# Performance work log

Measured on AMD Instinct MI355X. Metric: run time of the kernel, lower is better.

## Reference

```python
import jax, jax.numpy as jnp
import numpy as np

B, N, L, D, IN, H = 16, 100, 90, 300, 256, 256


def setup_inputs() -> dict:
    key = jax.random.key(0)
    ks = jax.random.split(key, 24)
    s = 0.02
    inp = {}
    inp["h_local"] = jax.random.normal(ks[0], (B, N, IN), jnp.float32)
    inp["items_review"] = jax.random.normal(ks[1], (B, N, L, D), jnp.float32)
    inp["adj_sg"] = jax.random.randint(ks[2], (B, N, 2 * N), 0, 2, jnp.int32)
    inp["attn_review_mask"] = jnp.zeros((B, N, L), jnp.bool_)
    # BatchNorm affine params (eval mode, running_mean=0, running_var=1)
    inp["bn_gamma"] = jnp.ones((IN,), jnp.float32)
    inp["bn_beta"] = jnp.zeros((IN,), jnp.float32)
    # MultiHeadAttention linear layers (review_dim=300)
    inp["W_q"] = jax.random.normal(ks[3], (D, D), jnp.float32) * s
    inp["b_q"] = jnp.zeros((D,), jnp.float32)
    inp["W_k"] = jax.random.normal(ks[4], (D, D), jnp.float32) * s
    inp["b_k"] = jnp.zeros((D,), jnp.float32)
    inp["W_v"] = jax.random.normal(ks[5], (D, D), jnp.float32) * s
    inp["b_v"] = jnp.zeros((D,), jnp.float32)
    inp["W_f"] = jax.random.normal(ks[6], (D, D), jnp.float32) * s
    inp["b_f"] = jnp.zeros((D,), jnp.float32)
    # fc: input_size -> hidden_size
    inp["W_fc"] = jax.random.normal(ks[7], (H, IN), jnp.float32) * s
    inp["b_fc"] = jnp.zeros((H,), jnp.float32)
    # edge linear layers
    inp["W_in"] = jax.random.normal(ks[8], (H, H), jnp.float32) * s
    inp["b_in"] = jnp.zeros((H,), jnp.float32)
    inp["W_out"] = jax.random.normal(ks[9], (H, H), jnp.float32) * s
    inp["b_out"] = jnp.zeros((H,), jnp.float32)
    inp["b_iah"] = jax.random.normal(ks[10], (H,), jnp.float32) * s
    inp["b_oah"] = jax.random.normal(ks[11], (H,), jnp.float32) * s
    # fc_in_out: 2H -> H
    inp["W_io"] = jax.random.normal(ks[12], (H, 2 * H), jnp.float32) * s
    inp["b_io"] = jnp.zeros((H,), jnp.float32)
    return inp


def reference(h_local, items_review, adj_sg, attn_review_mask,
              bn_gamma, bn_beta,
              W_q, b_q, W_k, b_k, W_v, b_v, W_f, b_f,
              W_fc, b_fc, W_in, b_in, W_out, b_out,
              b_iah, b_oah, W_io, b_io):
    n = h_local.shape[1]
    # BatchNorm1d (eval mode: running_mean=0, running_var=1) + fc
    h = h_local * (bn_gamma / jnp.sqrt(1.0 + 1e-5)) + bn_beta
    hidden = h @ W_fc.T + b_fc                                  # [B,N,H]

    # MultiHeadAttention over reviews (heads never split in original bmm)
    q = items_review @ W_q.T + b_q                              # [B,N,L,D]
    k = items_review @ W_k.T + b_k
    v = items_review @ W_v.T + b_v
    scale = (items_review.shape[-1] // 3) ** (-0.5)             # (300//3)^-0.5 = 0.1
    attn = jax.nn.softmax(jnp.einsum('bnld,bnmd->bnlm', q, k) * scale, axis=-1)
    ctx = jnp.einsum('bnlm,bnmd->bnld', attn, v)
    out_attn = items_review + (ctx @ W_f.T + b_f)               # residual
    h_review = jnp.sum(out_attn, axis=2)                        # [B,N,D] sum over review_len

    # pairwise cosine similarity (torch.cosine_similarity, eps=1e-8)
    norms = jnp.linalg.norm(h_review, axis=-1)                  # [B,N]
    sim = jnp.einsum('bnd,bmd->bnm', h_review, h_review) \
        / jnp.maximum(norms[:, :, None] * norms[:, None, :], 1e-8)

    adj_in = adj_sg[:, :, :n] > 0
    adj_out = adj_sg[:, :, n:2 * n] > 0
    NEG = jnp.float32(-9e15)
    sim_in = jax.nn.softmax(jnp.where(adj_in, sim, NEG), axis=-1)
    sim_out = jax.nn.softmax(jnp.where(adj_out, sim, NEG), axis=-1)

    input_in = jnp.einsum('bnm,bmh->bnh', sim_in, hidden @ W_in.T + b_in) + b_iah
    input_out = jnp.einsum('bnm,bmh->bnh', sim_out, hidden @ W_out.T + b_out) + b_oah
    output = jnp.concatenate([input_in, input_out], axis=-1) @ W_io.T + b_io
    return output
```

## Files before the change

### kernel.cpp

```cpp
#include <hip/hip_runtime.h>
#include <math.h>

#define Bb 16
#define Nn 100
#define Ll 90
#define Dd 300
#define NBLK (Bb*Nn)
#define LP 96
#define DP 320
#define DPH 40

typedef __attribute__((ext_vector_type(8))) short short8v;
typedef __attribute__((ext_vector_type(4))) short short4v;
typedef __attribute__((ext_vector_type(4))) float f32x4;

__device__ __forceinline__ unsigned short f2bf(float f) {
  unsigned int u = __float_as_uint(f);
  u += 0x7fffu + ((u >> 16) & 1u);
  return (unsigned short)(u >> 16);
}
__device__ __forceinline__ float bf2f(unsigned short h) {
  return __uint_as_float(((unsigned int)h) << 16);
}

__global__ __launch_bounds__(256) void k_setup(
    const float* __restrict__ Wq, const float* __restrict__ Wk,
    const float* __restrict__ bq, const float* __restrict__ bk,
    const float* __restrict__ Wf, const float* __restrict__ Wv,
    const float* __restrict__ bv, const float* __restrict__ bf,
    unsigned short* __restrict__ Mb, float* __restrict__ G,
    float* __restrict__ bias2) {
  int blk = blockIdx.x;
  if (blk < 400) {
    int idx = blk * 256 + threadIdx.x;
    int i = idx / DP, j = idx % DP;
    float s = 0.f;
    if (i <= Dd && j <= Dd) {
#pragma unroll 10
      for (int o = 0; o < Dd; o++) {
        float av = (i < Dd) ? Wq[o * Dd + i] : bq[o];
        float bw = (j < Dd) ? Wk[o * Dd + j] : bk[o];
        s += av * bw;
      }
    }
    Mb[idx] = f2bf(s);
  } else if (blk < 757) {
    int idx = (blk - 400) * 256 + threadIdx.x;
    if (idx < Dd * 304) {
      int o = idx / 304, p = idx % 304;
      float s = 0.f;
      if (p < Dd) {
#pragma unroll 10
        for (int v = 0; v < Dd; v++) s += Wf[o * Dd + v] * Wv[v * Dd + p];
      }
      G[idx] = s;
    }
  } else {
    for (int t = threadIdx.x; t < 304; t += 256) {
      float sb = 0.f;
      if (t < Dd) {
#pragma unroll 10
        for (int v = 0; v < Dd; v++) sb += Wf[t * Dd + v] * bv[v];
        sb = 90.f * (sb + bf[t]);
      }
      bias2[t] = sb;
    }
  }
}

__global__ __launch_bounds__(256) void k_mm256(
    const float* __restrict__ A0, const float* __restrict__ A1, int lda,
    const float* __restrict__ B0, const float* __restrict__ B1, int ldb,
    float* __restrict__ C, int ldc, const float* __restrict__ gamma) {
  const float* A = blockIdx.z ? A1 : A0;
  const float* B = blockIdx.z ? B1 : B0;
  float* Cb = C + (size_t)blockIdx.z * 256 * ldc;
  __shared__ float As[16][68];
  __shared__ float Bs[16][68];
  int m0 = blockIdx.x * 64, n0 = blockIdx.y * 64;
  int tx = threadIdx.x & 15, ty = threadIdx.x >> 4;
  float acc[4][4];
#pragma unroll
  for (int i = 0; i < 4; i++)
#pragma unroll
    for (int j = 0; j < 4; j++) acc[i][j] = 0.f;
  int r = threadIdx.x >> 2;
  int kq = (threadIdx.x & 3) << 2;
  int kk2 = threadIdx.x >> 4;
  int nq = (threadIdx.x & 15) << 2;
  for (int k0 = 0; k0 < 256; k0 += 16) {
    {
      float4 v = *(const float4*)(A + (size_t)(m0 + r) * lda + k0 + kq);
      As[kq + 0][r] = v.x; As[kq + 1][r] = v.y; As[kq + 2][r] = v.z; As[kq + 3][r] = v.w;
    }
    {
      float4 v = *(const float4*)(B + (size_t)(k0 + kk2) * ldb + n0 + nq);
      Bs[kk2][nq + 0] = v.x; Bs[kk2][nq + 1] = v.y; Bs[kk2][nq + 2] = v.z; Bs[kk2][nq + 3] = v.w;
    }
    __syncthreads();
#pragma unroll
    for (int kk = 0; kk < 16; kk++) {
      float4 av = *(const float4*)&As[kk][ty * 4];
      float4 bv = *(const float4*)&Bs[kk][tx * 4];
      acc[0][0] += av.x * bv.x; acc[0][1] += av.x * bv.y; acc[0][2] += av.x * bv.z; acc[0][3] += av.x * bv.w;
      acc[1][0] += av.y * bv.x; acc[1][1] += av.y * bv.y; acc[1][2] += av.y * bv.z; acc[1][3] += av.y * bv.w;
      acc[2][0] += av.z * bv.x; acc[2][1] += av.z * bv.y; acc[2][2] += av.z * bv.z; acc[2][3] += av.z * bv.w;
      acc[3][0] += av.w * bv.x; acc[3][1] += av.w * bv.y; acc[3][2] += av.w * bv.z; acc[3][3] += av.w * bv.w;
    }
    __syncthreads();
  }
  const float bninv = rsqrtf(1.00001f);
#pragma unroll
  for (int i = 0; i < 4; i++) {
    int gm = m0 + ty * 4 + i;
#pragma unroll
    for (int j = 0; j < 4; j++) {
      int gn = n0 + tx * 4 + j;
      float v = acc[i][j];
      if (gamma) v *= gamma[gn] * bninv;
      Cb[(size_t)gm * ldc + gn] = v;
    }
  }
}

__global__ __launch_bounds__(256) void k_vecd(
    const float* __restrict__ W_fc, const float* __restrict__ b_fc,
    const float* __restrict__ beta,
    const float* __restrict__ W_in, const float* __restrict__ b_in,
    const float* __restrict__ b_iah,
    const float* __restrict__ W_out, const float* __restrict__ b_out,
    const float* __restrict__ b_oah,
    const float* __restrict__ W_io, const float* __restrict__ b_io,
    float* __restrict__ dvec) {
  __shared__ float v1[256];
  __shared__ float v23[512];
  int i = threadIdx.x;
  float s = 0.f;
#pragma unroll 16
  for (int k = 0; k < 256; k++) s += W_fc[i * 256 + k] * beta[k];
  v1[i] = s + b_fc[i];
  __syncthreads();
  float s2 = 0.f, s3 = 0.f;
#pragma unroll 16
  for (int k = 0; k < 256; k++) {
    float vk = v1[k];
    s2 += W_in[i * 256 + k] * vk;
    s3 += W_out[i * 256 + k] * vk;
  }
  v23[i] = s2 + b_in[i] + b_iah[i];
  v23[256 + i] = s3 + b_out[i] + b_oah[i];
  __syncthreads();
  float sd = 0.f;
#pragma unroll 16
  for (int k = 0; k < 512; k++) sd += W_io[i * 512 + k] * v23[k];
  dvec[i] = sd + b_io[i];
}

__global__ __launch_bounds__(512, 4) void k_attn(
    const float* __restrict__ items, const unsigned short* __restrict__ Mb,
    float* __restrict__ r_all, float* __restrict__ colsum_all) {
  __shared__ unsigned short Xs[LP * DP];
  __shared__ unsigned short Zc[LP * 64];
  __shared__ float wsum[LP];

  const int tid = threadIdx.x;
  const int bid = blockIdx.x;
  const float* Xg = items + (size_t)bid * (Ll * Dd);

  if (tid < LP) wsum[tid] = 0.f;

  for (int c = tid; c < LP * DPH; c += 512) {
    int l = c / DPH, ch = c % DPH, d0 = ch * 8;
    float v[8];
    if (l < Ll && d0 < Dd) {
      if (d0 + 8 <= Dd) {
        float4 a = *(const float4*)(Xg + l * Dd + d0);
        float4 b = *(const float4*)(Xg + l * Dd + d0 + 4);
        v[0] = a.x; v[1] = a.y; v[2] = a.z; v[3] = a.w;
        v[4] = b.x; v[5] = b.y; v[6] = b.z; v[7] = b.w;
      } else {
#pragma unroll
        for (int q = 0; q < 8; q++) {
          int d = d0 + q;
          v[q] = (d < Dd) ? Xg[l * Dd + d] : ((d == Dd) ? 1.f : 0.f);
        }
      }
    } else {
#pragma unroll
      for (int q = 0; q < 8; q++) v[q] = 0.f;
    }
    short8v pk;
#pragma unroll
    for (int q = 0; q < 8; q++) pk[q] = (short)f2bf(v[q]);
    *(short8v*)((char*)Xs + l * 640 + ((d0 * 2) ^ ((l & 7) << 4))) = pk;
  }

  for (int d = tid; d < 304; d += 512) {
    float s = 0.f;
    if (d < Dd) {
#pragma unroll 18
      for (int l = 0; l < Ll; l++) s += Xg[l * Dd + d];
    }
    colsum_all[(size_t)bid * 304 + d] = s;
  }
  __syncthreads();

  const int lane = tid & 63, wave = tid >> 6;
  const int fr = lane & 15, kg = lane >> 4;

  int itile[3], bbyte[3], bswz[3], mrow[3], icol0[3];
#pragma unroll
  for (int tt = 0; tt < 3; tt++) {
    int t = wave + tt * 8;
    int ict = t / 6, mt = t - ict * 6;
    itile[tt] = ict * 16 + fr;
    int brow = mt * 16 + fr;
    bbyte[tt] = brow * 640;
    bswz[tt] = (brow & 7) << 4;
    mrow[tt] = brow;
    icol0[tt] = ict * 16 + kg * 4;
  }

  f32x4 acc[6];
#pragma unroll
  for (int mt = 0; mt < 6; mt++) acc[mt] = (f32x4){0.f, 0.f, 0.f, 0.f};

  for (int c = 0; c < 5; c++) {
    f32x4 z0 = (f32x4){0.f, 0.f, 0.f, 0.f}, z1 = z0, z2 = z0;
    const unsigned short* MbC = Mb + (size_t)(c * 64) * DP;
#pragma unroll
    for (int ks = 0; ks < 10; ks++) {
      int koff = ks * 32 + kg * 8;
      short8v a0 = *(const short8v*)(MbC + itile[0] * DP + koff);
      short8v b0 = *(const short8v*)((char*)Xs + bbyte[0] + ((koff * 2) ^ bswz[0]));
      z0 = __builtin_amdgcn_mfma_f32_16x16x32_bf16(a0, b0, z0, 0, 0, 0);
      short8v a1 = *(const short8v*)(MbC + itile[1] * DP + koff);
      short8v b1 = *(const short8v*)((char*)Xs + bbyte[1] + ((koff * 2) ^ bswz[1]));
      z1 = __builtin_amdgcn_mfma_f32_16x16x32_bf16(a1, b1, z1, 0, 0, 0);
      short8v a2 = *(const short8v*)(MbC + itile[2] * DP + koff);
      short8v b2 = *(const short8v*)((char*)Xs + bbyte[2] + ((koff * 2) ^ bswz[2]));
      z2 = __builtin_amdgcn_mfma_f32_16x16x32_bf16(a2, b2, z2, 0, 0, 0);
    }
#pragma unroll
    for (int tt = 0; tt < 3; tt++) {
      f32x4 z = tt == 0 ? z0 : (tt == 1 ? z1 : z2);
      short4v pk;
#pragma unroll
      for (int r2 = 0; r2 < 4; r2++) pk[r2] = (short)f2bf(z[r2]);
      *(short4v*)((char*)Zc + mrow[tt] * 128 +
                  ((icol0[tt] * 2) ^ ((mrow[tt] & 7) << 4))) = pk;
    }
    __syncthreads();
    if (wave < 6) {
      int arow = wave * 16 + fr;
      int abyte = arow * 640, aswz = (arow & 7) << 4;
#pragma unroll
      for (int mt = 0; mt < 6; mt++) {
        int brow = mt * 16 + fr;
#pragma unroll
        for (int ks = 0; ks < 2; ks++) {
          short8v a = *(const short8v*)((char*)Xs + abyte +
                                        (((c * 64 + ks * 32 + kg * 8) * 2) ^ aswz));
          short8v b = *(const short8v*)((char*)Zc + brow * 128 +
                                        (((ks * 32 + kg * 8) * 2) ^ ((brow & 7) << 4)));
          acc[mt] = __builtin_amdgcn_mfma_f32_16x16x32_bf16(a, b, acc[mt], 0, 0, 0);
        }
      }
    }
    __syncthreads();
  }

  if (wave < 6) {
    float colpart[6] = {0.f, 0.f, 0.f, 0.f, 0.f, 0.f};
#pragma unroll
    for (int r2 = 0; r2 < 4; r2++) {
      int l = wave * 16 + kg * 4 + r2;
      float x[6];
#pragma unroll
      for (int mt = 0; mt < 6; mt++) {
        int col = mt * 16 + fr;
        x[mt] = (col < Ll) ? 0.1f * acc[mt][r2] : -INFINITY;
      }
      float mx = x[0];
#pragma unroll
      for (int mt = 1; mt < 6; mt++) mx = fmaxf(mx, x[mt]);
      mx = fmaxf(mx, __shfl_xor(mx, 1));
      mx = fmaxf(mx, __shfl_xor(mx, 2));
      mx = fmaxf(mx, __shfl_xor(mx, 4));
      mx = fmaxf(mx, __shfl_xor(mx, 8));
      float e[6]; float s = 0.f;
#pragma unroll
      for (int mt = 0; mt < 6; mt++) { e[mt] = __expf(x[mt] - mx); s += e[mt]; }
      s += __shfl_xor(s, 1); s += __shfl_xor(s, 2);
      s += __shfl_xor(s, 4); s += __shfl_xor(s, 8);
      float inv = 1.f / s;
      if (l < Ll) {
#pragma unroll
        for (int mt = 0; mt < 6; mt++) colpart[mt] += e[mt] * inv;
      }
    }
#pragma unroll
    for (int mt = 0; mt < 6; mt++) {
      colpart[mt] += __shfl_xor(colpart[mt], 16);
      colpart[mt] += __shfl_xor(colpart[mt], 32);
    }
    if (lane < 16) {
#pragma unroll
      for (int mt = 0; mt < 6; mt++) atomicAdd(&wsum[mt * 16 + fr], colpart[mt]);
    }
  }
  __syncthreads();

  for (int i = tid; i < 304; i += 512) {
    float s = 0.f;
    if (i < Dd) {
#pragma unroll 15
      for (int m = 0; m < Ll; m++)
        s += wsum[m] * bf2f(Xs[(m * 640 + ((i * 2) ^ ((m & 7) << 4))) >> 1]);
    }
    r_all[(size_t)bid * 304 + i] = s;
  }
}

__global__ __launch_bounds__(256) void k_gemm_bt(
    const float* __restrict__ A, int lda, const float* __restrict__ W, int ldw,
    const float* __restrict__ bias, const float* __restrict__ res, int ldres,
    float* __restrict__ C, int ldc, int Mdim, int Ndim, int Kdim) {
  __shared__ float As[16][68];
  __shared__ float Bs[16][68];
  int m0 = blockIdx.x * 64, n0 = blockIdx.y * 64;
  int tx = threadIdx.x & 15, ty = threadIdx.x >> 4;
  float acc[4][4];
#pragma unroll
  for (int i = 0; i < 4; i++)
#pragma unroll
    for (int j = 0; j < 4; j++) acc[i][j] = 0.f;
  int r = threadIdx.x >> 2;
  int kq = (threadIdx.x & 3) << 2;
  for (int k0 = 0; k0 < Kdim; k0 += 16) {
    {
      int gm = m0 + r;
      float4 v = {0.f, 0.f, 0.f, 0.f};
      if (gm < Mdim) v = *(const float4*)(A + (size_t)gm * lda + k0 + kq);
      As[kq + 0][r] = v.x; As[kq + 1][r] = v.y; As[kq + 2][r] = v.z; As[kq + 3][r] = v.w;
    }
    {
      int gn = n0 + r;
      float4 v = {0.f, 0.f, 0.f, 0.f};
      if (gn < Ndim) v = *(const float4*)(W + (size_t)gn * ldw + k0 + kq);
      Bs[kq + 0][r] = v.x; Bs[kq + 1][r] = v.y; Bs[kq + 2][r] = v.z; Bs[kq + 3][r] = v.w;
    }
    __syncthreads();
#pragma unroll
    for (int kk = 0; kk < 16; kk++) {
      float4 av = *(const float4*)&As[kk][ty * 4];
      float4 bv = *(const float4*)&Bs[kk][tx * 4];
      acc[0][0] += av.x * bv.x; acc[0][1] += av.x * bv.y; acc[0][2] += av.x * bv.z; acc[0][3] += av.x * bv.w;
      acc[1][0] += av.y * bv.x; acc[1][1] += av.y * bv.y; acc[1][2] += av.y * bv.z; acc[1][3] += av.y * bv.w;
      acc[2][0] += av.z * bv.x; acc[2][1] += av.z * bv.y; acc[2][2] += av.z * bv.z; acc[2][3] += av.z * bv.w;
      acc[3][0] += av.w * bv.x; acc[3][1] += av.w * bv.y; acc[3][2] += av.w * bv.z; acc[3][3] += av.w * bv.w;
    }
    __syncthreads();
  }
#pragma unroll
  for (int i = 0; i < 4; i++) {
    int gm = m0 + ty * 4 + i;
    if (gm >= Mdim) continue;
#pragma unroll
    for (int j = 0; j < 4; j++) {
      int gn = n0 + tx * 4 + j;
      if (gn >= Ndim) continue;
      float v = acc[i][j];
      if (bias) v += bias[gn];
      if (res) v += res[(size_t)gm * ldres + gn];
      C[(size_t)gm * ldc + gn] = v;
    }
  }
}

__global__ __launch_bounds__(256) void k_norm(const float* __restrict__ hrev,
                                              unsigned short* __restrict__ Hn) {
  int row = blockIdx.x * 4 + (threadIdx.x >> 6);
  int lane = threadIdx.x & 63;
  float v[5]; float ss = 0.f;
#pragma unroll
  for (int j = 0; j < 5; j++) {
    int i = lane + j * 64;
    float x = (i < Dd) ? hrev[(size_t)row * 304 + i] : 0.f;
    v[j] = x; ss += x * x;
  }
#pragma unroll
  for (int o = 32; o; o >>= 1) ss += __shfl_xor(ss, o);
  float inv = (ss > 0.f) ? rsqrtf(ss) : 0.f;
#pragma unroll
  for (int j = 0; j < 5; j++) {
    int i = lane + j * 64;
    if (i < DP) Hn[(size_t)row * DP + i] = f2bf(v[j] * inv);
  }
}

__global__ __launch_bounds__(64) void k_simgram(
    const unsigned short* __restrict__ Hn, const int* __restrict__ adj,
    float* __restrict__ simin, float* __restrict__ simout) {
  int b = blockIdx.x, rt = blockIdx.y;
  int lane = threadIdx.x;
  int fr = lane & 15, kg = lane >> 4;
  const unsigned short* Hb = Hn + (size_t)b * Nn * DP;
  int ar = rt * 16 + fr;
  short8v zerov;
#pragma unroll
  for (int q = 0; q < 8; q++) zerov[q] = 0;
  f32x4 acc[7];
#pragma unroll
  for (int mt = 0; mt < 7; mt++) acc[mt] = (f32x4){0.f, 0.f, 0.f, 0.f};
#pragma unroll
  for (int ks = 0; ks < 10; ks++) {
    int koff = ks * 32 + kg * 8;
    short8v a = (ar < Nn) ? *(const short8v*)(Hb + (size_t)ar * DP + koff) : zerov;
#pragma unroll
    for (int mt = 0; mt < 7; mt++) {
      int br = mt * 16 + fr;
      short8v bb = (br < Nn) ? *(const short8v*)(Hb + (size_t)br * DP + koff) : zerov;
      acc[mt] = __builtin_amdgcn_mfma_f32_16x16x32_bf16(a, bb, acc[mt], 0, 0, 0);
    }
  }
  const int* adjb = adj + (size_t)b * Nn * 2 * Nn;
#pragma unroll
  for (int which = 0; which < 2; which++) {
    float* dst = which ? simout : simin;
#pragma unroll
    for (int r2 = 0; r2 < 4; r2++) {
      int l = rt * 16 + kg * 4 + r2;
      bool lv = l < Nn;
      float x[7];
#pragma unroll
      for (int mt = 0; mt < 7; mt++) {
        int col = mt * 16 + fr;
        bool cvd = col < Nn;
        int am = (lv && cvd) ? adjb[l * (2 * Nn) + which * Nn + col] : 0;
        x[mt] = cvd ? ((am > 0) ? acc[mt][r2] : -9e15f) : -INFINITY;
      }
      float mx = x[0];
#pragma unroll
      for (int mt = 1; mt < 7; mt++) mx = fmaxf(mx, x[mt]);
      mx = fmaxf(mx, __shfl_xor(mx, 1));
      mx = fmaxf(mx, __shfl_xor(mx, 2));
      mx = fmaxf(mx, __shfl_xor(mx, 4));
      mx = fmaxf(mx, __shfl_xor(mx, 8));
      float e[7]; float s = 0.f;
#pragma unroll
      for (int mt = 0; mt < 7; mt++) { e[mt] = __expf(x[mt] - mx); s += e[mt]; }
      s += __shfl_xor(s, 1); s += __shfl_xor(s, 2);
      s += __shfl_xor(s, 4); s += __shfl_xor(s, 8);
      float inv = 1.f / s;
      if (lv) {
#pragma unroll
        for (int mt = 0; mt < 7; mt++) {
          int col = mt * 16 + fr;
          if (col < Nn) dst[((size_t)(b * Nn + l)) * Nn + col] = e[mt] * inv;
        }
      }
    }
  }
}

__global__ __launch_bounds__(256) void k_mixout(
    const float* __restrict__ simin, const float* __restrict__ simout,
    const float* __restrict__ P, const float* __restrict__ dvec,
    float* __restrict__ out) {
  __shared__ float si[Nn], so[Nn];
  int bn = blockIdx.x, h = threadIdx.x, b = bn / Nn;
  if (h < Nn) {
    si[h] = simin[(size_t)bn * Nn + h];
    so[h] = simout[(size_t)bn * Nn + h];
  }
  __syncthreads();
  const float* Pb = P + (size_t)b * Nn * 512;
  float acc = dvec[h];
#pragma unroll 10
  for (int m = 0; m < Nn; m++)
    acc += si[m] * Pb[m * 512 + h] + so[m] * Pb[m * 512 + 256 + h];
  out[(size_t)bn * 256 + h] = acc;
}

extern "C" void kernel_launch(void* const* d_in, const int* in_sizes, int n_in,
                              void* d_out, int out_size, void* d_ws, size_t ws_size,
                              hipStream_t stream) {
  (void)in_sizes; (void)n_in; (void)out_size; (void)ws_size;
  const float* h_local = (const float*)d_in[0];
  const float* items   = (const float*)d_in[1];
  const int*   adj     = (const int*)d_in[2];
  const float* bn_g  = (const float*)d_in[4];
  const float* bn_b  = (const float*)d_in[5];
  const float* W_q = (const float*)d_in[6];   const float* b_q = (const float*)d_in[7];
  const float* W_k = (const float*)d_in[8];   const float* b_k = (const float*)d_in[9];
  const float* W_v = (const float*)d_in[10];  const float* b_v = (const float*)d_in[11];
  const float* W_f = (const float*)d_in[12];  const float* b_f = (const float*)d_in[13];
  const float* W_fc = (const float*)d_in[14]; const float* b_fc = (const float*)d_in[15];
  const float* W_in = (const float*)d_in[16]; const float* b_in = (const float*)d_in[17];
  const float* W_out = (const float*)d_in[18]; const float* b_out = (const float*)d_in[19];
  const float* b_iah = (const float*)d_in[20]; const float* b_oah = (const float*)d_in[21];
  const float* W_io = (const float*)d_in[22];  const float* b_io = (const float*)d_in[23];
  float* out = (float*)d_out;

  char* w = (char*)d_ws;
  auto alloc = [&](size_t bytes) { char* p = w; w += (bytes + 255) & ~(size_t)255; return p; };
  unsigned short* Mb = (unsigned short*)alloc((size_t)DP * DP * 2);
  float* G      = (float*)alloc((size_t)Dd * 304 * 4);
  float* bias2  = (float*)alloc(304 * 4);
  float* Tbuf   = (float*)alloc((size_t)512 * 256 * 4);
  float* Bcat   = (float*)alloc((size_t)512 * 256 * 4);
  float* dvec   = (float*)alloc(256 * 4);
  float* r_all  = (float*)alloc((size_t)NBLK * 304 * 4);
  float* colsum = (float*)alloc((size_t)NBLK * 304 * 4);
  float* hrev   = (float*)alloc((size_t)NBLK * 304 * 4);
  unsigned short* Hn = (unsigned short*)alloc((size_t)NBLK * DP * 2);
  float* simin  = (float*)alloc((size_t)NBLK * Nn * 4);
  float* simout = (float*)alloc((size_t)NBLK * Nn * 4);
  float* P      = (float*)alloc((size_t)NBLK * 512 * 4);

  k_setup<<<758, 256, 0, stream>>>(W_q, W_k, b_q, b_k, W_f, W_v, b_v, b_f,
                                   Mb, G, bias2);
  k_attn<<<NBLK, 512, 0, stream>>>(items, Mb, r_all, colsum);

  {
    dim3 g(4, 4, 2);
    k_mm256<<<g, 256, 0, stream>>>(W_in, W_out, 256, W_fc, W_fc, 256, Tbuf, 256, nullptr);
    k_mm256<<<g, 256, 0, stream>>>(W_io, W_io + 256, 512, Tbuf, Tbuf + 256 * 256, 256,
                                   Bcat, 256, bn_g);
  }
  k_vecd<<<1, 256, 0, stream>>>(W_fc, b_fc, bn_b, W_in, b_in, b_iah,
                                W_out, b_out, b_oah, W_io, b_io, dvec);
  {
    dim3 g(25, 8);
    k_gemm_bt<<<g, 256, 0, stream>>>(h_local, 256, Bcat, 256, nullptr, nullptr, 0,
                                     P, 512, NBLK, 512, 256);
  }
  {
    dim3 g(25, 5);
    k_gemm_bt<<<g, 256, 0, stream>>>(r_all, 304, G, 304, bias2, colsum, 304,
                                     hrev, 304, NBLK, 300, 304);
  }
  k_norm<<<NBLK / 4, 256, 0, stream>>>(hrev, Hn);
  {
    dim3 g(Bb, 7);
    k_simgram<<<g, 64, 0, stream>>>(Hn, adj, simin, simout);
  }
  k_mixout<<<NBLK, 256, 0, stream>>>(simin, simout, P, dvec, out);
}
```

Measured before the change: 747.2 us.

## Split attention kernel into Z-projection and score/softmax kernels via global ZT buffer

Splits the fused attention kernel in two. The first kernel computes Z = M·X^T for each block (all 20 row tiles at once, no chunked LDS ping-pong) and writes it to a global bf16 workspace. The second kernel, at 384 threads, reads X straight from global and ZT to form the scores, softmax and weighted sum. This removes the per-chunk syncthreads and the LDS-staged second GEMM, at the cost of about 98 MB of extra global write and read traffic and one more launch. The old fused kernel remains as a fallback when the workspace is too small.

```diff
diff --git a/kernel.cpp b/kernel.cpp
--- a/kernel.cpp
+++ b/kernel.cpp
@@ -156,18 +156,13 @@
   dvec[i] = sd + b_io[i];
 }
 
-__global__ __launch_bounds__(512, 4) void k_attn(
+__global__ __launch_bounds__(512, 4) void k_zt(
     const float* __restrict__ items, const unsigned short* __restrict__ Mb,
-    float* __restrict__ r_all, float* __restrict__ colsum_all) {
+    unsigned short* __restrict__ ZT, float* __restrict__ colsum_all) {
   __shared__ unsigned short Xs[LP * DP];
-  __shared__ unsigned short Zc[LP * 64];
-  __shared__ float wsum[LP];
-
   const int tid = threadIdx.x;
   const int bid = blockIdx.x;
   const float* Xg = items + (size_t)bid * (Ll * Dd);
-
-  if (tid < LP) wsum[tid] = 0.f;
 
   for (int c = tid; c < LP * DPH; c += 512) {
     int l = c / DPH, ch = c % DPH, d0 = ch * 8;
@@ -194,6 +189,38 @@
     for (int q = 0; q < 8; q++) pk[q] = (short)f2bf(v[q]);
     *(short8v*)((char*)Xs + l * 640 + ((d0 * 2) ^ ((l & 7) << 4))) = pk;
   }
+  __syncthreads();
+
+  const int lane = tid & 63, wave = tid >> 6;
+  const int fr = lane & 15, kg = lane >> 4;
+  unsigned short* ZTb = ZT + (size_t)bid * (LP * DP);
+
+  for (int t = wave; t < 20; t += 8) {
+    f32x4 z[6];
+#pragma unroll
+    for (int mt = 0; mt < 6; mt++) z[mt] = (f32x4){0.f, 0.f, 0.f, 0.f};
+    const unsigned short* Ma = Mb + (size_t)(t * 16 + fr) * DP;
+#pragma unroll
+    for (int ks = 0; ks < 10; ks++) {
+      int koff = ks * 32 + kg * 8;
+      short8v a = *(const short8v*)(Ma + koff);
+#pragma unroll
+      for (int mt = 0; mt < 6; mt++) {
+        int brow = mt * 16 + fr;
+        short8v b = *(const short8v*)((char*)Xs + brow * 640 +
+                                      ((koff * 2) ^ ((brow & 7) << 4)));
+        z[mt] = __builtin_amdgcn_mfma_f32_16x16x32_bf16(a, b, z[mt], 0, 0, 0);
+      }
+    }
+#pragma unroll
+    for (int mt = 0; mt < 6; mt++) {
+      int m = mt * 16 + fr;
+      short4v pk;
+#pragma unroll
+      for (int r2 = 0; r2 < 4; r2++) pk[r2] = (short)f2bf(z[mt][r2]);
+      *(short4v*)(ZTb + (size_t)m * DP + t * 16 + kg * 4) = pk;
+    }
+  }
 
   for (int d = tid; d < 304; d += 512) {
     float s = 0.f;
@@ -203,52 +230,178 @@
     }
     colsum_all[(size_t)bid * 304 + d] = s;
   }
-  __syncthreads();
-
+}
+
+__global__ __launch_bounds__(384, 4) void k_attn2(
+    const float* __restrict__ items, const unsigned short* __restrict__ ZT,
+    float* __restrict__ r_all) {
+  __shared__ float wsum[LP];
+  const int tid = threadIdx.x;
+  const int bid = blockIdx.x;
   const int lane = tid & 63, wave = tid >> 6;
   const int fr = lane & 15, kg = lane >> 4;
-
-  int itile[3], bbyte[3], bswz[3], mrow[3], icol0[3];
-#pragma unroll
-  for (int tt = 0; tt < 3; tt++) {
-    int t = wave + tt * 8;
-    int ict = t / 6, mt = t - ict * 6;
-    itile[tt] = ict * 16 + fr;
-    int brow = mt * 16 + fr;
-    bbyte[tt] = brow * 640;
-    bswz[tt] = (brow & 7) << 4;
-    mrow[tt] = brow;
-    icol0[tt] = ict * 16 + kg * 4;
-  }
+  if (tid < LP) wsum[tid] = 0.f;
+  __syncthreads();
+
+  const float* Xg = items + (size_t)bid * (Ll * Dd);
+  const unsigned short* ZTb = ZT + (size_t)bid * (LP * DP);
 
   f32x4 acc[6];
 #pragma unroll
   for (int mt = 0; mt < 6; mt++) acc[mt] = (f32x4){0.f, 0.f, 0.f, 0.f};
 
+  const int l = wave * 16 + fr;
+  const bool lval = l < Ll;
+  const float* Xrow = Xg + (size_t)l * Dd;
+
+#pragma unroll
+  for (int ks = 0; ks < 10; ks++) {
+    int k0 = ks * 32 + kg * 8;
+    short8v a;
+    if (lval && k0 + 8 <= Dd) {
+      float4 f0 = *(const float4*)(Xrow + k0);
+      float4 f1 = *(const float4*)(Xrow + k0 + 4);
+      a[0] = (short)f2bf(f0.x); a[1] = (short)f2bf(f0.y);
+      a[2] = (short)f2bf(f0.z); a[3] = (short)f2bf(f0.w);
+      a[4] = (short)f2bf(f1.x); a[5] = (short)f2bf(f1.y);
+      a[6] = (short)f2bf(f1.z); a[7] = (short)f2bf(f1.w);
+    } else if (lval && k0 < Dd) {
+      float4 f0 = *(const float4*)(Xrow + k0);
+      a[0] = (short)f2bf(f0.x); a[1] = (short)f2bf(f0.y);
+      a[2] = (short)f2bf(f0.z); a[3] = (short)f2bf(f0.w);
+      a[4] = (short)0x3F80; a[5] = 0; a[6] = 0; a[7] = 0;
+    } else {
+#pragma unroll
+      for (int q = 0; q < 8; q++) a[q] = 0;
+    }
+#pragma unroll
+    for (int mt = 0; mt < 6; mt++) {
+      int brow = mt * 16 + fr;
+      short8v b = *(const short8v*)(ZTb + (size_t)brow * DP + k0);
+      acc[mt] = __builtin_amdgcn_mfma_f32_16x16x32_bf16(a, b, acc[mt], 0, 0, 0);
+    }
+  }
+
+  {
+    float colpart[6] = {0.f, 0.f, 0.f, 0.f, 0.f, 0.f};
+#pragma unroll
+    for (int r2 = 0; r2 < 4; r2++) {
+      int lr = wave * 16 + kg * 4 + r2;
+      float x[6];
+#pragma unroll
+      for (int mt = 0; mt < 6; mt++) {
+        int col = mt * 16 + fr;
+        x[mt] = (col < Ll) ? 0.1f * acc[mt][r2] : -INFINITY;
+      }
+      float mx = x[0];
+#pragma unroll
+      for (int mt = 1; mt < 6; mt++) mx = fmaxf(mx, x[mt]);
+      mx = fmaxf(mx, __shfl_xor(mx, 1));
+      mx = fmaxf(mx, __shfl_xor(mx, 2));
+      mx = fmaxf(mx, __shfl_xor(mx, 4));
+      mx = fmaxf(mx, __shfl_xor(mx, 8));
+      float e[6]; float s = 0.f;
+#pragma unroll
+      for (int mt = 0; mt < 6; mt++) { e[mt] = __expf(x[mt] - mx); s += e[mt]; }
+      s += __shfl_xor(s, 1); s += __shfl_xor(s, 2);
+      s += __shfl_xor(s, 4); s += __shfl_xor(s, 8);
+      float inv = 1.f / s;
+      if (lr < Ll) {
+#pragma unroll
+        for (int mt = 0; mt < 6; mt++) colpart[mt] += e[mt] * inv;
+      }
+    }
+#pragma unroll
+    for (int mt = 0; mt < 6; mt++) {
+      colpart[mt] += __shfl_xor(colpart[mt], 16);
+      colpart[mt] += __shfl_xor(colpart[mt], 32);
+    }
+    if (lane < 16) {
+#pragma unroll
+      for (int mt = 0; mt < 6; mt++) atomicAdd(&wsum[mt * 16 + fr], colpart[mt]);
+    }
+  }
+  __syncthreads();
+
+  for (int i = tid; i < 304; i += 384) {
+    float s = 0.f;
+    if (i < Dd) {
+#pragma unroll 15
+      for (int m = 0; m < Ll; m++) s += wsum[m] * Xg[(size_t)m * Dd + i];
+    }
+    r_all[(size_t)bid * 304 + i] = s;
+  }
+}
+
+__global__ __launch_bounds__(512, 4) void k_attn(
+    const float* __restrict__ items, const unsigned short* __restrict__ Mb,
+    float* __restrict__ r_all, float* __restrict__ colsum_all) {
+  __shared__ unsigned short Xs[LP * DP];
+  __shared__ unsigned short Zc[LP * 64];
+  __shared__ float wsum[LP];
+  const int tid = threadIdx.x;
+  const int bid = blockIdx.x;
+  const float* Xg = items + (size_t)bid * (Ll * Dd);
+  if (tid < LP) wsum[tid] = 0.f;
+  for (int c = tid; c < LP * DPH; c += 512) {
+    int l = c / DPH, ch = c % DPH, d0 = ch * 8;
+    float v[8];
+    if (l < Ll && d0 < Dd) {
+      if (d0 + 8 <= Dd) {
+        float4 a = *(const float4*)(Xg + l * Dd + d0);
+        float4 b = *(const float4*)(Xg + l * Dd + d0 + 4);
+        v[0] = a.x; v[1] = a.y; v[2] = a.z; v[3] = a.w;
+        v[4] = b.x; v[5] = b.y; v[6] = b.z; v[7] = b.w;
+      } else {
+#pragma unroll
+        for (int q = 0; q < 8; q++) {
+          int d = d0 + q;
+          v[q] = (d < Dd) ? Xg[l * Dd + d] : ((d == Dd) ? 1.f : 0.f);
+        }
+      }
+    } else {
+#pragma unroll
+      for (int q = 0; q < 8; q++) v[q] = 0.f;
+    }
+    short8v pk;
+#pragma unroll
+    for (int q = 0; q < 8; q++) pk[q] = (short)f2bf(v[q]);
+    *(short8v*)((char*)Xs + l * 640 + ((d0 * 2) ^ ((l & 7) << 4))) = pk;
+  }
+  for (int d = tid; d < 304; d += 512) {
+    float s = 0.f;
+    if (d < Dd) {
+#pragma unroll 18
+      for (int l = 0; l < Ll; l++) s += Xg[l * Dd + d];
+    }
+    colsum_all[(size_t)bid * 304 + d] = s;
+  }
+  __syncthreads();
+  const int lane = tid & 63, wave = tid >> 6;
+  const int fr = lane & 15, kg = lane >> 4;
+  f32x4 acc[6];
+#pragma unroll
+  for (int mt = 0; mt < 6; mt++) acc[mt] = (f32x4){0.f, 0.f, 0.f, 0.f};
   for (int c = 0; c < 5; c++) {
-    f32x4 z0 = (f32x4){0.f, 0.f, 0.f, 0.f}, z1 = z0, z2 = z0;
-    const unsigned short* MbC = Mb + (size_t)(c * 64) * DP;
-#pragma unroll
-    for (int ks = 0; ks < 10; ks++) {
-      int koff = ks * 32 + kg * 8;
-      short8v a0 = *(const short8v*)(MbC + itile[0] * DP + koff);
-      short8v b0 = *(const short8v*)((char*)Xs + bbyte[0] + ((koff * 2) ^ bswz[0]));
-      z0 = __builtin_amdgcn_mfma_f32_16x16x32_bf16(a0, b0, z0, 0, 0, 0);
-      short8v a1 = *(const short8v*)(MbC + itile[1] * DP + koff);
-      short8v b1 = *(const short8v*)((char*)Xs + bbyte[1] + ((koff * 2) ^ bswz[1]));
-      z1 = __builtin_amdgcn_mfma_f32_16x16x32_bf16(a1, b1, z1, 0, 0, 0);
-      short8v a2 = *(const short8v*)(MbC + itile[2] * DP + koff);
-      short8v b2 = *(const short8v*)((char*)Xs + bbyte[2] + ((koff * 2) ^ bswz[2]));
-      z2 = __builtin_amdgcn_mfma_f32_16x16x32_bf16(a2, b2, z2, 0, 0, 0);
-    }
-#pragma unroll
-    for (int tt = 0; tt < 3; tt++) {
-      f32x4 z = tt == 0 ? z0 : (tt == 1 ? z1 : z2);
+    for (int t = wave; t < 24; t += 8) {
+      int ict = t / 6, mt = t - ict * 6;
+      int irow = c * 64 + ict * 16 + fr;
+      f32x4 zacc = (f32x4){0.f, 0.f, 0.f, 0.f};
+#pragma unroll
+      for (int ks = 0; ks < 10; ks++) {
+        int koff = ks * 32 + kg * 8;
+        short8v a = *(const short8v*)(Mb + (size_t)irow * DP + koff);
+        int brow = mt * 16 + fr;
+        short8v b = *(const short8v*)((char*)Xs + brow * 640 +
+                                      ((koff * 2) ^ ((brow & 7) << 4)));
+        zacc = __builtin_amdgcn_mfma_f32_16x16x32_bf16(a, b, zacc, 0, 0, 0);
+      }
+      int m = mt * 16 + fr;
+      int ic0 = ict * 16 + kg * 4;
       short4v pk;
 #pragma unroll
-      for (int r2 = 0; r2 < 4; r2++) pk[r2] = (short)f2bf(z[r2]);
-      *(short4v*)((char*)Zc + mrow[tt] * 128 +
-                  ((icol0[tt] * 2) ^ ((mrow[tt] & 7) << 4))) = pk;
+      for (int r2 = 0; r2 < 4; r2++) pk[r2] = (short)f2bf(zacc[r2]);
+      *(short4v*)((char*)Zc + m * 128 + ((ic0 * 2) ^ ((m & 7) << 4))) = pk;
     }
     __syncthreads();
     if (wave < 6) {
@@ -269,7 +422,6 @@
     }
     __syncthreads();
   }
-
   if (wave < 6) {
     float colpart[6] = {0.f, 0.f, 0.f, 0.f, 0.f, 0.f};
 #pragma unroll
@@ -310,7 +462,6 @@
     }
   }
   __syncthreads();
-
   for (int i = tid; i < 304; i += 512) {
     float s = 0.f;
     if (i < Dd) {
@@ -486,7 +637,7 @@
 extern "C" void kernel_launch(void* const* d_in, const int* in_sizes, int n_in,
                               void* d_out, int out_size, void* d_ws, size_t ws_size,
                               hipStream_t stream) {
-  (void)in_sizes; (void)n_in; (void)out_size; (void)ws_size;
+  (void)in_sizes; (void)n_in; (void)out_size;
   const float* h_local = (const float*)d_in[0];
   const float* items   = (const float*)d_in[1];
   const int*   adj     = (const int*)d_in[2];
@@ -518,10 +669,17 @@
   float* simin  = (float*)alloc((size_t)NBLK * Nn * 4);
   float* simout = (float*)alloc((size_t)NBLK * Nn * 4);
   float* P      = (float*)alloc((size_t)NBLK * 512 * 4);
+  unsigned short* ZT = (unsigned short*)alloc((size_t)NBLK * LP * DP * 2);
+  const bool big = ((size_t)(w - (char*)d_ws)) <= ws_size;
 
   k_setup<<<758, 256, 0, stream>>>(W_q, W_k, b_q, b_k, W_f, W_v, b_v, b_f,
                                    Mb, G, bias2);
-  k_attn<<<NBLK, 512, 0, stream>>>(items, Mb, r_all, colsum);
+  if (big) {
+    k_zt<<<NBLK, 512, 0, stream>>>(items, Mb, ZT, colsum);
+    k_attn2<<<NBLK, 384, 0, stream>>>(items, ZT, r_all);
+  } else {
+    k_attn<<<NBLK, 512, 0, stream>>>(items, Mb, r_all, colsum);
+  }
 
   {
     dim3 g(4, 4, 2);
```

After: 990.2 us. +32.5%, slower.
